# Kernel tuning notes

Hardware: AMD Instinct MI355X
Metric: run time of the kernel (lower is better)

Reference implementation:

```python
import jax, jax.numpy as jnp
import numpy as np
from jax import lax

B, T, IN, H, OUT, L = 256, 200, 128, 256, 118, 2


def _gru_layer(x_seq, Wih, Whh, bih, bhh):
    """x_seq: [B, T, D] -> all hidden states [B, T, H] (PyTorch GRU gate math)."""
    # Precompute input contribution to gates for all timesteps: [B, T, 3H]
    gx_all = jnp.einsum('btd,gd->btg', x_seq, Wih) + bih

    def step(h, gx):
        gh = h @ Whh.T + bhh                      # [B, 3H]
        r = jax.nn.sigmoid(gx[:, :H] + gh[:, :H])
        z = jax.nn.sigmoid(gx[:, H:2 * H] + gh[:, H:2 * H])
        n = jnp.tanh(gx[:, 2 * H:] + r * gh[:, 2 * H:])
        h_new = (1.0 - z) * n + z * h
        return h_new, h_new

    h0 = jnp.zeros((x_seq.shape[0], H), dtype=x_seq.dtype)
    _, hs = lax.scan(step, h0, gx_all.swapaxes(0, 1))  # hs: [T, B, H]
    return hs.swapaxes(0, 1)


def setup_inputs() -> dict:
    key = jax.random.key(0)
    ks = jax.random.split(key, 11)
    s_in = 1.0 / np.sqrt(H)
    u = lambda k, shp: jax.random.uniform(k, shp, jnp.float32, -s_in, s_in)
    return {
        'x':    jax.random.normal(ks[0], (B, T, IN), jnp.float32),
        'Wih0': u(ks[1], (3 * H, IN)),
        'Whh0': u(ks[2], (3 * H, H)),
        'bih0': u(ks[3], (3 * H,)),
        'bhh0': u(ks[4], (3 * H,)),
        'Wih1': u(ks[5], (3 * H, H)),
        'Whh1': u(ks[6], (3 * H, H)),
        'bih1': u(ks[7], (3 * H,)),
        'bhh1': u(ks[8], (3 * H,)),
        'fcW':  u(ks[9], (OUT, H)),
        'fcb':  u(ks[10], (OUT,)),
    }


def reference(x, Wih0, Whh0, bih0, bhh0, Wih1, Whh1, bih1, bhh1, fcW, fcb):
    h1 = _gru_layer(x, Wih0, Whh0, bih0, bhh0)   # [B, T, H]
    h2 = _gru_layer(h1, Wih1, Whh1, bih1, bhh1)  # [B, T, H]
    last = h2[:, -1, :]                           # out[:, -1, :]
    return last @ fcW.T + fcb                     # [B, OUT]
```

## Files before the change

kernel.cpp:

```cpp
#include <hip/hip_runtime.h>
#include <hip/hip_bf16.h>
#include <stdint.h>

#define BATCH 256
#define SEQT  200
#define IND   128
#define HID   256
#define G3    768
#define OUTD  118

#define TC    25
#define NC    8

#define HSTRIDE 264
#define W0SZ (G3*IND)
#define WHSZ (G3*HID)
#define XSZ  (BATCH*SEQT*IND)

#define SLOT_F  (BATCH*TC*G3)
#define SLOTP_F (SLOT_F + 2048)

#define NLOG2E (-1.44269504f)
#define LOG2E2 2.88539008f

typedef short  short8 __attribute__((ext_vector_type(8)));
typedef float  f32x4  __attribute__((ext_vector_type(4)));
typedef int    i32x4  __attribute__((ext_vector_type(4)));

__device__ __forceinline__ float exp2fast(float x) {
#if __has_builtin(__builtin_amdgcn_exp2f)
    return __builtin_amdgcn_exp2f(x);
#else
    return exp2f(x);
#endif
}

__device__ __forceinline__ unsigned short f2bf(float x) {
    union { float f; uint32_t u; } v; v.f = x;
    uint32_t u = v.u;
    u += 0x7FFF + ((u >> 16) & 1);
    return (unsigned short)(u >> 16);
}

__device__ __forceinline__ void scan_barrier() {
    asm volatile("s_waitcnt lgkmcnt(0)" ::: "memory");
    __builtin_amdgcn_s_barrier();
    __builtin_amdgcn_sched_barrier(0);
}

__global__ void cvt_all(const float* __restrict__ x,
                        const float* __restrict__ w0,  const float* __restrict__ wh0,
                        const float* __restrict__ w1,  const float* __restrict__ wh1,
                        unsigned short* __restrict__ xb,
                        unsigned short* __restrict__ o0,  unsigned short* __restrict__ oh0,
                        unsigned short* __restrict__ o1,  unsigned short* __restrict__ oh1) {
    const int n4 = (XSZ + W0SZ + 3 * WHSZ) / 4;
    int idx = blockIdx.x * blockDim.x + threadIdx.x;
    int stride = gridDim.x * blockDim.x;
    for (int i = idx; i < n4; i += stride) {
        int j = i * 4;
        const float* src; unsigned short* dst;
        if (j < XSZ) { src = x; dst = xb; }
        else {
            j -= XSZ;
            if (j < W0SZ) { src = w0; dst = o0; }
            else {
                j -= W0SZ;
                if (j < WHSZ) { src = wh0; dst = oh0; }
                else {
                    j -= WHSZ;
                    if (j < WHSZ) { src = w1; dst = o1; }
                    else { j -= WHSZ; src = wh1; dst = oh1; }
                }
            }
        }
        float4 v = *(const float4*)(src + j);
        ushort4 o;
        o.x = f2bf(v.x); o.y = f2bf(v.y); o.z = f2bf(v.z); o.w = f2bf(v.w);
        *(ushort4*)(dst + j) = o;
    }
}

__global__ void combine_bias(const float* __restrict__ bih0, const float* __restrict__ bhh0,
                             const float* __restrict__ bih1, const float* __restrict__ bhh1,
                             float* __restrict__ bc0, float* __restrict__ bc1) {
    int i = blockIdx.x * blockDim.x + threadIdx.x;
    if (i < G3) bc0[i] = bih0[i] + (i < 2 * HID ? bhh0[i] : 0.0f);
    else if (i < 2 * G3) {
        int j = i - G3;
        bc1[j] = bih1[j] + (j < 2 * HID ? bhh1[j] : 0.0f);
    }
}

template<int K>
__device__ __forceinline__ void g_stage(i32x4* sA, int tile, int t0,
    const unsigned short* A, const unsigned short* Bt, const float* bias,
    int tidu, short8 (&b)[2][8], float& bia0, float& bia1, int& g0o)
{
    constexpr int KS = K / 32, CPR = K / 8, LSTR = CPR + 1, PT = 128 * CPR / 256;
    const int wave = tidu >> 6, lane = tidu & 63, col = lane & 15, quad = lane >> 4;
    const int nb = tile % 6, panel = tile / 6;
    const int g0 = nb * 128 + wave * 32 + col;
    g0o = g0;
#pragma unroll
    for (int jt = 0; jt < 2; jt++)
#pragma unroll
        for (int ks = 0; ks < KS; ks++)
            b[jt][ks] = *(const short8*)(Bt + (size_t)(g0 + jt * 16) * K + ks * 32 + quad * 8);
    bia0 = bias[g0]; bia1 = bias[g0 + 16];

    i32x4 st[PT];
#pragma unroll
    for (int i = 0; i < PT; i++) {
        int g = i * 256 + tidu;
        int row = g / CPR, cc = g % CPR;
        int r = panel * 128 + row;
        int bb = r / TC, lt = r - bb * TC;
        st[i] = *(const i32x4*)(A + (size_t)(bb * SEQT + t0 + lt) * K + cc * 8);
    }
#pragma unroll
    for (int i = 0; i < PT; i++) {
        int g = i * 256 + tidu;
        sA[(g / CPR) * LSTR + (g % CPR)] = st[i];
    }
}

template<int K>
__device__ __forceinline__ void g_comp(const i32x4* sA, int tile,
    const short8 (&b)[2][8], float bia0, float bia1, int g0,
    float* Cslot, int tidu)
{
    constexpr int KS = K / 32, CPR = K / 8, LSTR = CPR + 1;
    const int lane = tidu & 63, col = lane & 15, quad = lane >> 4;
    const int nb = tile % 6, panel = tile / 6;
    const float scl = (nb < 4) ? NLOG2E : LOG2E2;
#pragma unroll 2
    for (int ms = 0; ms < 8; ms++) {
        f32x4 a0 = (f32x4)(0.0f), a1 = (f32x4)(0.0f);
#pragma unroll
        for (int ks = 0; ks < KS; ks++) {
            short8 a = __builtin_bit_cast(short8, sA[(ms * 16 + col) * LSTR + ks * 4 + quad]);
            a0 = __builtin_amdgcn_mfma_f32_16x16x32_bf16(a, b[0][ks], a0, 0, 0, 0);
            a1 = __builtin_amdgcn_mfma_f32_16x16x32_bf16(a, b[1][ks], a1, 0, 0, 0);
        }
        float* crow = Cslot + (size_t)(panel * 128 + ms * 16 + quad * 4) * G3 + g0;
#pragma unroll
        for (int r = 0; r < 4; r++) {
            crow[(size_t)r * G3]      = (a0[r] + bia0) * scl;
            crow[(size_t)r * G3 + 16] = (a1[r] + bia1) * scl;
        }
    }
}

__global__ __launch_bounds__(512, 2) void pipe(
    int c,
    const unsigned short* xb,
    unsigned short* h1b,
    const unsigned short* w0b, const unsigned short* w1b,
    const float* bc0, const float* bc1,
    float* gx0, float* gx1,
    const unsigned short* wh0, const unsigned short* wh1,
    const float* bhh0, const float* bhh1,
    float* hst0, float* hst1)
{
    __shared__ __attribute__((aligned(16))) char SM[16896 + 135168];

    const int bid = blockIdx.x;
    const int tid = threadIdx.x;

    if (bid < 128) {
        const bool L0 = bid < 64;
        const int cs = L0 ? c - 1 : c - 3;
        if (cs < 0 || cs >= NC) return;
        const float* gxslot = (L0 ? gx0 : gx1) + (size_t)(cs & 1) * SLOTP_F;
        const unsigned short* Whh = L0 ? wh0 : wh1;
        const float* bhh = L0 ? bhh0 : bhh1;
        float* hstate = L0 ? hst0 : hst1;
        unsigned short* h1o = L0 ? h1b : nullptr;
        const int wg = L0 ? bid : bid - 64;

        unsigned short* hs = (unsigned short*)SM;

        const int wave = tid >> 6, lane = tid & 63;
        const int col = lane & 15, quad = lane >> 4;
        const int jbase = wave * 32, j0 = jbase + col, j1 = jbase + 16 + col;
        const int bq  = wg * 4 + quad;
        const int row = quad * 4;

        i32x4 wrz[2][2][8];
#pragma unroll
        for (int g = 0; g < 2; g++)
#pragma unroll
            for (int jt = 0; jt < 2; jt++)
#pragma unroll
                for (int ks = 0; ks < 8; ks++)
                    wrz[g][jt][ks] = *(const i32x4*)(
                        Whh + (size_t)(g * HID + jbase + jt * 16 + col) * HID + ks * 32 + quad * 8);
        i32x4 wn0[8], wn1r[8];
#pragma unroll
        for (int ks = 0; ks < 8; ks++) {
            wn0[ks]  = *(const i32x4*)(Whh + (size_t)(2 * HID + j0) * HID + ks * 32 + quad * 8);
            wn1r[ks] = *(const i32x4*)(Whh + (size_t)(2 * HID + j1) * HID + ks * 32 + quad * 8);
        }

        for (int i = tid; i < 2 * 16 * HSTRIDE; i += 512) hs[i] = 0;

        float hreg[2];
        if (cs == 0) { hreg[0] = 0.0f; hreg[1] = 0.0f; }
        else {
            hreg[0] = hstate[bq * HID + j0];
            hreg[1] = hstate[bq * HID + j1];
        }
        float bhn[2] = { bhh[2 * HID + j0], bhh[2 * HID + j1] };

        __syncthreads();
        hs[row * HSTRIDE + j0] = f2bf(hreg[0]);
        hs[row * HSTRIDE + j1] = f2bf(hreg[1]);
        __syncthreads();

        int gof = (bq * TC) * G3 + j0;
        int hof = (bq * SEQT + cs * TC) * HID + j0;
        const int abase = col * HSTRIDE + quad * 8;
        const int wbase = row * HSTRIDE + j0;

        float gc[3][2], gc1[3][2], gc2[3][2];
#pragma unroll
        for (int g3 = 0; g3 < 3; g3++) {
            gc[g3][0] = gxslot[gof + g3 * HID];
            gc[g3][1] = gxslot[gof + g3 * HID + 16];
        }
        gof += G3;
#pragma unroll
        for (int g3 = 0; g3 < 3; g3++) {
            gc1[g3][0] = gxslot[gof + g3 * HID];
            gc1[g3][1] = gxslot[gof + g3 * HID + 16];
        }
        gof += G3;

        for (int lt = 0; lt < TC; lt++) {
            unsigned short* hc = hs + (lt & 1) * 16 * HSTRIDE;
            unsigned short* hn = hs + ((lt & 1) ^ 1) * 16 * HSTRIDE;

#pragma unroll
            for (int g = 0; g < 2; g++)
#pragma unroll
                for (int jt = 0; jt < 2; jt++)
#pragma unroll
                    for (int ks = 0; ks < 8; ks++)
                        asm volatile("" : "+v"(wrz[g][jt][ks]));
#pragma unroll
            for (int ks = 0; ks < 8; ks++) {
                asm volatile("" : "+v"(wn0[ks]));
                asm volatile("" : "+v"(wn1r[ks]));
            }

#pragma unroll
            for (int g3 = 0; g3 < 3; g3++) {
                gc2[g3][0] = gxslot[gof + g3 * HID];
                gc2[g3][1] = gxslot[gof + g3 * HID + 16];
            }
            gof += G3;

            f32x4 acc[3][2];
#pragma unroll
            for (int g = 0; g < 3; g++)
#pragma unroll
                for (int jt = 0; jt < 2; jt++) acc[g][jt] = (f32x4)(0.0f);

            __builtin_amdgcn_s_setprio(1);
#pragma unroll
            for (int ks = 0; ks < 8; ks++) {
                short8 a = *(const short8*)(&hc[abase + ks * 32]);
                acc[0][0] = __builtin_amdgcn_mfma_f32_16x16x32_bf16(a, __builtin_bit_cast(short8, wrz[0][0][ks]), acc[0][0], 0, 0, 0);
                acc[0][1] = __builtin_amdgcn_mfma_f32_16x16x32_bf16(a, __builtin_bit_cast(short8, wrz[0][1][ks]), acc[0][1], 0, 0, 0);
                acc[1][0] = __builtin_amdgcn_mfma_f32_16x16x32_bf16(a, __builtin_bit_cast(short8, wrz[1][0][ks]), acc[1][0], 0, 0, 0);
                acc[1][1] = __builtin_amdgcn_mfma_f32_16x16x32_bf16(a, __builtin_bit_cast(short8, wrz[1][1][ks]), acc[1][1], 0, 0, 0);
                acc[2][0] = __builtin_amdgcn_mfma_f32_16x16x32_bf16(a, __builtin_bit_cast(short8, wn0[ks]),       acc[2][0], 0, 0, 0);
                acc[2][1] = __builtin_amdgcn_mfma_f32_16x16x32_bf16(a, __builtin_bit_cast(short8, wn1r[ks]),      acc[2][1], 0, 0, 0);
            }
            __builtin_amdgcn_s_setprio(0);

            unsigned short hb[2];
#pragma unroll
            for (int jt = 0; jt < 2; jt++) {
                float er = exp2fast(__builtin_fmaf(acc[0][jt][0], NLOG2E, gc[0][jt]));
                float rr = __builtin_amdgcn_rcpf(1.0f + er);
                float ez = exp2fast(__builtin_fmaf(acc[1][jt][0], NLOG2E, gc[1][jt]));
                float zz = __builtin_amdgcn_rcpf(1.0f + ez);
                float inner = acc[2][jt][0] + bhn[jt];
                float en = exp2fast(__builtin_fmaf(rr * inner, LOG2E2, gc[2][jt]));
                float nn = __builtin_fmaf(__builtin_amdgcn_rcpf(1.0f + en), -2.0f, 1.0f);
                float hnew = __builtin_fmaf(zz, hreg[jt] - nn, nn);
                hreg[jt] = hnew;
                hb[jt] = f2bf(hnew);
                hn[wbase + jt * 16] = hb[jt];
            }

            if (h1o) {
                h1o[hof]      = hb[0];
                h1o[hof + 16] = hb[1];
            }
            hof += HID;

#pragma unroll
            for (int g3 = 0; g3 < 3; g3++) {
                gc[g3][0]  = gc1[g3][0];  gc[g3][1]  = gc1[g3][1];
                gc1[g3][0] = gc2[g3][0];  gc1[g3][1] = gc2[g3][1];
            }

            scan_barrier();
        }

        hstate[bq * HID + j0] = hreg[0];
        hstate[bq * HID + j1] = hreg[1];

    } else {
        const int cg0 = c, cg1 = c - 2;
        const int G0t = (cg0 < NC) ? 300 : 0;
        const int G1t = (cg1 >= 0 && cg1 < NC) ? 300 : 0;
        if (G0t + G1t == 0) return;

        i32x4* sA = (i32x4*)(SM + 16896) + (tid >> 8) * 4224;
        const int u    = (bid - 128) * 2 + (tid >> 8);
        const int tidu = tid & 255;
        float* c0slot = gx0 + (size_t)(cg0 & 1) * SLOTP_F;
        float* c1slot = gx1 + (size_t)(cg1 & 1) * SLOTP_F;

        short8 bf[2][8];
        float bia0, bia1; int g0c;

#pragma unroll 1
        for (int it = 0; it < 3; it++) {
            int t = it * 256 + u;
            int mode = (t < G0t) ? 0 : ((t - G0t < G1t) ? 1 : -1);
            int tile = (mode == 1) ? t - G0t : t;
            if (mode == 0)
                g_stage<IND>(sA, tile, cg0 * TC, xb, w0b, bc0, tidu, bf, bia0, bia1, g0c);
            else if (mode == 1)
                g_stage<HID>(sA, tile, cg1 * TC, h1b, w1b, bc1, tidu, bf, bia0, bia1, g0c);
            __syncthreads();
            if (mode == 0)
                g_comp<IND>(sA, tile, bf, bia0, bia1, g0c, c0slot, tidu);
            else if (mode == 1)
                g_comp<HID>(sA, tile, bf, bia0, bia1, g0c, c1slot, tidu);
            __syncthreads();
        }
    }
}

__global__ __launch_bounds__(128) void fc_kernel(
    const float* __restrict__ hlast, const float* __restrict__ W,
    const float* __restrict__ b, float* __restrict__ out)
{
    __shared__ float hsm[HID];
    int bidx = blockIdx.x;
    for (int i = threadIdx.x; i < HID; i += 128) hsm[i] = hlast[(size_t)bidx * HID + i];
    __syncthreads();
    int o = threadIdx.x;
    if (o < OUTD) {
        float acc = b[o];
        const float* wrow = W + (size_t)o * HID;
#pragma unroll 4
        for (int k = 0; k < HID; k++) acc += hsm[k] * wrow[k];
        out[(size_t)bidx * OUTD + o] = acc;
    }
}

extern "C" void kernel_launch(void* const* d_in, const int* in_sizes, int n_in,
                              void* d_out, int out_size, void* d_ws, size_t ws_size,
                              hipStream_t stream) {
    const float* x    = (const float*)d_in[0];
    const float* Wih0 = (const float*)d_in[1];
    const float* Whh0 = (const float*)d_in[2];
    const float* bih0 = (const float*)d_in[3];
    const float* bhh0 = (const float*)d_in[4];
    const float* Wih1 = (const float*)d_in[5];
    const float* Whh1 = (const float*)d_in[6];
    const float* bih1 = (const float*)d_in[7];
    const float* bhh1 = (const float*)d_in[8];
    const float* fcW  = (const float*)d_in[9];
    const float* fcb  = (const float*)d_in[10];
    float* out = (float*)d_out;

    char* ws = (char*)d_ws;
    size_t off = 0;
    auto walloc = [&](size_t bytes) {
        void* p = ws + off;
        off = (off + bytes + 255) & ~(size_t)255;
        return p;
    };

    const int M = BATCH * SEQT;
    unsigned short* xb   = (unsigned short*)walloc((size_t)XSZ * 2);
    float*          gx0  = (float*)         walloc((size_t)2 * SLOTP_F * 4);
    float*          gx1  = (float*)         walloc((size_t)2 * SLOTP_F * 4);
    unsigned short* h1b  = (unsigned short*)walloc((size_t)M * HID * 2);
    unsigned short* w0b  = (unsigned short*)walloc((size_t)W0SZ * 2);
    unsigned short* wh0b = (unsigned short*)walloc((size_t)WHSZ * 2);
    unsigned short* w1b  = (unsigned short*)walloc((size_t)WHSZ * 2);
    unsigned short* wh1b = (unsigned short*)walloc((size_t)WHSZ * 2);
    float*          bc0  = (float*)         walloc(G3 * 4);
    float*          bc1  = (float*)         walloc(G3 * 4);
    float*          hst0 = (float*)         walloc((size_t)BATCH * HID * 4);
    float*          hst1 = (float*)         walloc((size_t)BATCH * HID * 4);

    cvt_all     <<<2048, 256, 0, stream>>>(x, Wih0, Whh0, Wih1, Whh1,
                                           xb, w0b, wh0b, w1b, wh1b);
    combine_bias<<<6,    256, 0, stream>>>(bih0, bhh0, bih1, bhh1, bc0, bc1);

    for (int c = 0; c <= NC + 2; ++c)
        pipe<<<256, 512, 0, stream>>>(c, xb, h1b, w0b, w1b, bc0, bc1,
                                      gx0, gx1, wh0b, wh1b, bhh0, bhh1, hst0, hst1);

    fc_kernel<<<BATCH, 128, 0, stream>>>(hst1, fcW, fcb, out);
}
```

Baseline: 506.9 us.

## Replace per-chunk kernel launches with persistent kernel using flag-based inter-block sync

Folds the eleven chunk-pipeline launches into one persistent kernel. Recurrence blocks keep their hidden state and weights in registers across chunks. Blocks coordinate through global atomic counters: recurrence blocks spin until the input-projection tiles for their chunk are published, and GEMM blocks wait for the h1 and slot-reuse completion counts before writing. This removes launch gaps and the hidden-state save/restore through global memory between chunks. In exchange it adds spin-wait latency and coherent atomic loads, and it relies on all 256 blocks being co-resident to avoid deadlock.

```diff
diff --git a/kernel.cpp b/kernel.cpp
--- a/kernel.cpp
+++ b/kernel.cpp
@@ -11,6 +11,7 @@
 
 #define TC    25
 #define NC    8
+#define G0TILES 300
 
 #define HSTRIDE 264
 #define W0SZ (G3*IND)
@@ -19,6 +20,11 @@
 
 #define SLOT_F  (BATCH*TC*G3)
 #define SLOTP_F (SLOT_F + 2048)
+
+#define FH1 0
+#define FS1 8
+#define FG0 16
+#define FG1 24
 
 #define NLOG2E (-1.44269504f)
 #define LOG2E2 2.88539008f
@@ -48,14 +54,28 @@
     __builtin_amdgcn_sched_barrier(0);
 }
 
+__device__ __forceinline__ void spin_ge(int* p, int tgt) {
+    while (__hip_atomic_load(p, __ATOMIC_ACQUIRE, __HIP_MEMORY_SCOPE_AGENT) < tgt)
+        __builtin_amdgcn_s_sleep(2);
+}
+
+__device__ __forceinline__ float gloadf(const float* p) {
+    return __hip_atomic_load(p, __ATOMIC_RELAXED, __HIP_MEMORY_SCOPE_AGENT);
+}
+__device__ __forceinline__ uint32_t gloadu(const uint32_t* p) {
+    return __hip_atomic_load(p, __ATOMIC_RELAXED, __HIP_MEMORY_SCOPE_AGENT);
+}
+
 __global__ void cvt_all(const float* __restrict__ x,
                         const float* __restrict__ w0,  const float* __restrict__ wh0,
                         const float* __restrict__ w1,  const float* __restrict__ wh1,
                         unsigned short* __restrict__ xb,
                         unsigned short* __restrict__ o0,  unsigned short* __restrict__ oh0,
-                        unsigned short* __restrict__ o1,  unsigned short* __restrict__ oh1) {
+                        unsigned short* __restrict__ o1,  unsigned short* __restrict__ oh1,
+                        int* __restrict__ flg) {
     const int n4 = (XSZ + W0SZ + 3 * WHSZ) / 4;
     int idx = blockIdx.x * blockDim.x + threadIdx.x;
+    if (idx < 32) flg[idx] = 0;
     int stride = gridDim.x * blockDim.x;
     for (int i = idx; i < n4; i += stride) {
         int j = i * 4;
@@ -92,7 +112,7 @@
     }
 }
 
-template<int K>
+template<int K, bool COH>
 __device__ __forceinline__ void g_stage(i32x4* sA, int tile, int t0,
     const unsigned short* A, const unsigned short* Bt, const float* bias,
     int tidu, short8 (&b)[2][8], float& bia0, float& bia1, int& g0o)
@@ -116,7 +136,18 @@
         int row = g / CPR, cc = g % CPR;
         int r = panel * 128 + row;
         int bb = r / TC, lt = r - bb * TC;
-        st[i] = *(const i32x4*)(A + (size_t)(bb * SEQT + t0 + lt) * K + cc * 8);
+        const unsigned short* src = A + (size_t)(bb * SEQT + t0 + lt) * K + cc * 8;
+        if constexpr (COH) {
+            const uint32_t* q = (const uint32_t*)src;
+            i32x4 v;
+            v[0] = (int)gloadu(q + 0);
+            v[1] = (int)gloadu(q + 1);
+            v[2] = (int)gloadu(q + 2);
+            v[3] = (int)gloadu(q + 3);
+            st[i] = v;
+        } else {
+            st[i] = *(const i32x4*)src;
+        }
     }
 #pragma unroll
     for (int i = 0; i < PT; i++) {
@@ -152,8 +183,7 @@
     }
 }
 
-__global__ __launch_bounds__(512, 2) void pipe(
-    int c,
+__global__ __launch_bounds__(512, 2) void persist(
     const unsigned short* xb,
     unsigned short* h1b,
     const unsigned short* w0b, const unsigned short* w1b,
@@ -161,7 +191,7 @@
     float* gx0, float* gx1,
     const unsigned short* wh0, const unsigned short* wh1,
     const float* bhh0, const float* bhh1,
-    float* hst0, float* hst1)
+    float* hlast, int* flg)
 {
     __shared__ __attribute__((aligned(16))) char SM[16896 + 135168];
 
@@ -170,14 +200,13 @@
 
     if (bid < 128) {
         const bool L0 = bid < 64;
-        const int cs = L0 ? c - 1 : c - 3;
-        if (cs < 0 || cs >= NC) return;
-        const float* gxslot = (L0 ? gx0 : gx1) + (size_t)(cs & 1) * SLOTP_F;
         const unsigned short* Whh = L0 ? wh0 : wh1;
         const float* bhh = L0 ? bhh0 : bhh1;
-        float* hstate = L0 ? hst0 : hst1;
+        float* gxb = L0 ? gx0 : gx1;
         unsigned short* h1o = L0 ? h1b : nullptr;
         const int wg = L0 ? bid : bid - 64;
+        int* fgx   = flg + (L0 ? FG0 : FG1);
+        int* fdone = flg + (L0 ? FH1 : FS1);
 
         unsigned short* hs = (unsigned short*)SM;
 
@@ -205,145 +234,174 @@
 
         for (int i = tid; i < 2 * 16 * HSTRIDE; i += 512) hs[i] = 0;
 
-        float hreg[2];
-        if (cs == 0) { hreg[0] = 0.0f; hreg[1] = 0.0f; }
-        else {
-            hreg[0] = hstate[bq * HID + j0];
-            hreg[1] = hstate[bq * HID + j1];
-        }
+        float hreg[2] = { 0.0f, 0.0f };
         float bhn[2] = { bhh[2 * HID + j0], bhh[2 * HID + j1] };
-
-        __syncthreads();
-        hs[row * HSTRIDE + j0] = f2bf(hreg[0]);
-        hs[row * HSTRIDE + j1] = f2bf(hreg[1]);
-        __syncthreads();
-
-        int gof = (bq * TC) * G3 + j0;
-        int hof = (bq * SEQT + cs * TC) * HID + j0;
         const int abase = col * HSTRIDE + quad * 8;
         const int wbase = row * HSTRIDE + j0;
 
-        float gc[3][2], gc1[3][2], gc2[3][2];
-#pragma unroll
-        for (int g3 = 0; g3 < 3; g3++) {
-            gc[g3][0] = gxslot[gof + g3 * HID];
-            gc[g3][1] = gxslot[gof + g3 * HID + 16];
-        }
-        gof += G3;
-#pragma unroll
-        for (int g3 = 0; g3 < 3; g3++) {
-            gc1[g3][0] = gxslot[gof + g3 * HID];
-            gc1[g3][1] = gxslot[gof + g3 * HID + 16];
-        }
-        gof += G3;
-
-        for (int lt = 0; lt < TC; lt++) {
-            unsigned short* hc = hs + (lt & 1) * 16 * HSTRIDE;
-            unsigned short* hn = hs + ((lt & 1) ^ 1) * 16 * HSTRIDE;
-
-#pragma unroll
-            for (int g = 0; g < 2; g++)
-#pragma unroll
-                for (int jt = 0; jt < 2; jt++)
-#pragma unroll
-                    for (int ks = 0; ks < 8; ks++)
-                        asm volatile("" : "+v"(wrz[g][jt][ks]));
-#pragma unroll
-            for (int ks = 0; ks < 8; ks++) {
-                asm volatile("" : "+v"(wn0[ks]));
-                asm volatile("" : "+v"(wn1r[ks]));
-            }
-
+        __syncthreads();
+
+        int cur = 0;
+        for (int c = 0; c < NC; ++c) {
+            if (tid == 0) spin_ge(&fgx[c], G0TILES);
+            __syncthreads();
+
+            const float* gxslot = gxb + (size_t)(c & 1) * SLOTP_F;
+            int gof = (bq * TC) * G3 + j0;
+            int hof = (bq * SEQT + c * TC) * HID + j0;
+
+            float gc[3][2], gc1[3][2], gc2[3][2];
 #pragma unroll
             for (int g3 = 0; g3 < 3; g3++) {
-                gc2[g3][0] = gxslot[gof + g3 * HID];
-                gc2[g3][1] = gxslot[gof + g3 * HID + 16];
+                gc[g3][0] = gloadf(gxslot + gof + g3 * HID);
+                gc[g3][1] = gloadf(gxslot + gof + g3 * HID + 16);
             }
             gof += G3;
-
-            f32x4 acc[3][2];
-#pragma unroll
-            for (int g = 0; g < 3; g++)
-#pragma unroll
-                for (int jt = 0; jt < 2; jt++) acc[g][jt] = (f32x4)(0.0f);
-
-            __builtin_amdgcn_s_setprio(1);
-#pragma unroll
-            for (int ks = 0; ks < 8; ks++) {
-                short8 a = *(const short8*)(&hc[abase + ks * 32]);
-                acc[0][0] = __builtin_amdgcn_mfma_f32_16x16x32_bf16(a, __builtin_bit_cast(short8, wrz[0][0][ks]), acc[0][0], 0, 0, 0);
-                acc[0][1] = __builtin_amdgcn_mfma_f32_16x16x32_bf16(a, __builtin_bit_cast(short8, wrz[0][1][ks]), acc[0][1], 0, 0, 0);
-                acc[1][0] = __builtin_amdgcn_mfma_f32_16x16x32_bf16(a, __builtin_bit_cast(short8, wrz[1][0][ks]), acc[1][0], 0, 0, 0);
-                acc[1][1] = __builtin_amdgcn_mfma_f32_16x16x32_bf16(a, __builtin_bit_cast(short8, wrz[1][1][ks]), acc[1][1], 0, 0, 0);
-                acc[2][0] = __builtin_amdgcn_mfma_f32_16x16x32_bf16(a, __builtin_bit_cast(short8, wn0[ks]),       acc[2][0], 0, 0, 0);
-                acc[2][1] = __builtin_amdgcn_mfma_f32_16x16x32_bf16(a, __builtin_bit_cast(short8, wn1r[ks]),      acc[2][1], 0, 0, 0);
-            }
-            __builtin_amdgcn_s_setprio(0);
-
-            unsigned short hb[2];
-#pragma unroll
-            for (int jt = 0; jt < 2; jt++) {
-                float er = exp2fast(__builtin_fmaf(acc[0][jt][0], NLOG2E, gc[0][jt]));
-                float rr = __builtin_amdgcn_rcpf(1.0f + er);
-                float ez = exp2fast(__builtin_fmaf(acc[1][jt][0], NLOG2E, gc[1][jt]));
-                float zz = __builtin_amdgcn_rcpf(1.0f + ez);
-                float inner = acc[2][jt][0] + bhn[jt];
-                float en = exp2fast(__builtin_fmaf(rr * inner, LOG2E2, gc[2][jt]));
-                float nn = __builtin_fmaf(__builtin_amdgcn_rcpf(1.0f + en), -2.0f, 1.0f);
-                float hnew = __builtin_fmaf(zz, hreg[jt] - nn, nn);
-                hreg[jt] = hnew;
-                hb[jt] = f2bf(hnew);
-                hn[wbase + jt * 16] = hb[jt];
-            }
-
-            if (h1o) {
-                h1o[hof]      = hb[0];
-                h1o[hof + 16] = hb[1];
-            }
-            hof += HID;
-
 #pragma unroll
             for (int g3 = 0; g3 < 3; g3++) {
-                gc[g3][0]  = gc1[g3][0];  gc[g3][1]  = gc1[g3][1];
-                gc1[g3][0] = gc2[g3][0];  gc1[g3][1] = gc2[g3][1];
-            }
-
-            scan_barrier();
-        }
-
-        hstate[bq * HID + j0] = hreg[0];
-        hstate[bq * HID + j1] = hreg[1];
+                gc1[g3][0] = gloadf(gxslot + gof + g3 * HID);
+                gc1[g3][1] = gloadf(gxslot + gof + g3 * HID + 16);
+            }
+            gof += G3;
+
+            for (int lt = 0; lt < TC; lt++) {
+                unsigned short* hc = hs + cur * 16 * HSTRIDE;
+                unsigned short* hn = hs + (cur ^ 1) * 16 * HSTRIDE;
+
+#pragma unroll
+                for (int g = 0; g < 2; g++)
+#pragma unroll
+                    for (int jt = 0; jt < 2; jt++)
+#pragma unroll
+                        for (int ks = 0; ks < 8; ks++)
+                            asm volatile("" : "+v"(wrz[g][jt][ks]));
+#pragma unroll
+                for (int ks = 0; ks < 8; ks++) {
+                    asm volatile("" : "+v"(wn0[ks]));
+                    asm volatile("" : "+v"(wn1r[ks]));
+                }
+
+#pragma unroll
+                for (int g3 = 0; g3 < 3; g3++) {
+                    gc2[g3][0] = gloadf(gxslot + gof + g3 * HID);
+                    gc2[g3][1] = gloadf(gxslot + gof + g3 * HID + 16);
+                }
+                gof += G3;
+
+                f32x4 acc[3][2];
+#pragma unroll
+                for (int g = 0; g < 3; g++)
+#pragma unroll
+                    for (int jt = 0; jt < 2; jt++) acc[g][jt] = (f32x4)(0.0f);
+
+                __builtin_amdgcn_s_setprio(1);
+#pragma unroll
+                for (int ks = 0; ks < 8; ks++) {
+                    short8 a = *(const short8*)(&hc[abase + ks * 32]);
+                    acc[0][0] = __builtin_amdgcn_mfma_f32_16x16x32_bf16(a, __builtin_bit_cast(short8, wrz[0][0][ks]), acc[0][0], 0, 0, 0);
+                    acc[0][1] = __builtin_amdgcn_mfma_f32_16x16x32_bf16(a, __builtin_bit_cast(short8, wrz[0][1][ks]), acc[0][1], 0, 0, 0);
+                    acc[1][0] = __builtin_amdgcn_mfma_f32_16x16x32_bf16(a, __builtin_bit_cast(short8, wrz[1][0][ks]), acc[1][0], 0, 0, 0);
+                    acc[1][1] = __builtin_amdgcn_mfma_f32_16x16x32_bf16(a, __builtin_bit_cast(short8, wrz[1][1][ks]), acc[1][1], 0, 0, 0);
+                    acc[2][0] = __builtin_amdgcn_mfma_f32_16x16x32_bf16(a, __builtin_bit_cast(short8, wn0[ks]),       acc[2][0], 0, 0, 0);
+                    acc[2][1] = __builtin_amdgcn_mfma_f32_16x16x32_bf16(a, __builtin_bit_cast(short8, wn1r[ks]),      acc[2][1], 0, 0, 0);
+                }
+                __builtin_amdgcn_s_setprio(0);
+
+                unsigned short hb[2];
+#pragma unroll
+                for (int jt = 0; jt < 2; jt++) {
+                    float er = exp2fast(__builtin_fmaf(acc[0][jt][0], NLOG2E, gc[0][jt]));
+                    float rr = __builtin_amdgcn_rcpf(1.0f + er);
+                    float ez = exp2fast(__builtin_fmaf(acc[1][jt][0], NLOG2E, gc[1][jt]));
+                    float zz = __builtin_amdgcn_rcpf(1.0f + ez);
+                    float inner = acc[2][jt][0] + bhn[jt];
+                    float en = exp2fast(__builtin_fmaf(rr * inner, LOG2E2, gc[2][jt]));
+                    float nn = __builtin_fmaf(__builtin_amdgcn_rcpf(1.0f + en), -2.0f, 1.0f);
+                    float hnew = __builtin_fmaf(zz, hreg[jt] - nn, nn);
+                    hreg[jt] = hnew;
+                    hb[jt] = f2bf(hnew);
+                    hn[wbase + jt * 16] = hb[jt];
+                }
+
+                if (h1o) {
+                    h1o[hof]      = hb[0];
+                    h1o[hof + 16] = hb[1];
+                }
+                hof += HID;
+
+#pragma unroll
+                for (int g3 = 0; g3 < 3; g3++) {
+                    gc[g3][0]  = gc1[g3][0];  gc[g3][1]  = gc1[g3][1];
+                    gc1[g3][0] = gc2[g3][0];  gc1[g3][1] = gc2[g3][1];
+                }
+
+                cur ^= 1;
+                scan_barrier();
+            }
+
+            __threadfence();
+            __syncthreads();
+            if (tid == 0)
+                __hip_atomic_fetch_add(&fdone[c], 1, __ATOMIC_RELEASE, __HIP_MEMORY_SCOPE_AGENT);
+        }
+
+        if (!L0) {
+            hlast[bq * HID + j0]      = hreg[0];
+            hlast[bq * HID + j0 + 16] = hreg[1];
+        }
 
     } else {
-        const int cg0 = c, cg1 = c - 2;
-        const int G0t = (cg0 < NC) ? 300 : 0;
-        const int G1t = (cg1 >= 0 && cg1 < NC) ? 300 : 0;
-        if (G0t + G1t == 0) return;
-
+        const int g  = bid - 128;
+        const int uu = g * 2 + (tid >> 8);
+        const int tidu = tid & 255;
+        const int ub = uu * G0TILES / 256;
+        const int ue = (uu + 1) * G0TILES / 256;
         i32x4* sA = (i32x4*)(SM + 16896) + (tid >> 8) * 4224;
-        const int u    = (bid - 128) * 2 + (tid >> 8);
-        const int tidu = tid & 255;
-        float* c0slot = gx0 + (size_t)(cg0 & 1) * SLOTP_F;
-        float* c1slot = gx1 + (size_t)(cg1 & 1) * SLOTP_F;
+
+        const int blkTiles = ((g * 2 + 2) * G0TILES / 256) - ((g * 2) * G0TILES / 256);
 
         short8 bf[2][8];
         float bia0, bia1; int g0c;
 
+        for (int cc = 0; cc < NC + 2; ++cc) {
+            const int c0 = cc, c1 = cc - 2;
+            const bool do0 = (c0 < NC), do1 = (c1 >= 0);
+
+            if (tid == 0) {
+                if (do0 && c0 >= 2) spin_ge(&flg[FH1 + c0 - 2], 64);
+                if (do1) {
+                    spin_ge(&flg[FH1 + c1], 64);
+                    if (c1 >= 2) spin_ge(&flg[FS1 + c1 - 2], 64);
+                }
+            }
+            __syncthreads();
+
+            float* s0 = gx0 + (size_t)(c0 & 1) * SLOTP_F;
+            float* s1 = gx1 + (size_t)(c1 & 1) * SLOTP_F;
+
 #pragma unroll 1
-        for (int it = 0; it < 3; it++) {
-            int t = it * 256 + u;
-            int mode = (t < G0t) ? 0 : ((t - G0t < G1t) ? 1 : -1);
-            int tile = (mode == 1) ? t - G0t : t;
-            if (mode == 0)
-                g_stage<IND>(sA, tile, cg0 * TC, xb, w0b, bc0, tidu, bf, bia0, bia1, g0c);
-            else if (mode == 1)
-                g_stage<HID>(sA, tile, cg1 * TC, h1b, w1b, bc1, tidu, bf, bia0, bia1, g0c);
+            for (int r = 0; r < 2; ++r) {
+                int t = ub + r; bool act = do0 && (t < ue);
+                if (act) g_stage<IND, false>(sA, t, c0 * TC, xb, w0b, bc0, tidu, bf, bia0, bia1, g0c);
+                __syncthreads();
+                if (act) g_comp<IND>(sA, t, bf, bia0, bia1, g0c, s0, tidu);
+                __syncthreads();
+            }
+#pragma unroll 1
+            for (int r = 0; r < 2; ++r) {
+                int t = ub + r; bool act = do1 && (t < ue);
+                if (act) g_stage<HID, true>(sA, t, c1 * TC, h1b, w1b, bc1, tidu, bf, bia0, bia1, g0c);
+                __syncthreads();
+                if (act) g_comp<HID>(sA, t, bf, bia0, bia1, g0c, s1, tidu);
+                __syncthreads();
+            }
+
+            __threadfence();
             __syncthreads();
-            if (mode == 0)
-                g_comp<IND>(sA, tile, bf, bia0, bia1, g0c, c0slot, tidu);
-            else if (mode == 1)
-                g_comp<HID>(sA, tile, bf, bia0, bia1, g0c, c1slot, tidu);
-            __syncthreads();
+            if (tid == 0) {
+                if (do0) __hip_atomic_fetch_add(&flg[FG0 + c0], blkTiles, __ATOMIC_RELEASE, __HIP_MEMORY_SCOPE_AGENT);
+                if (do1) __hip_atomic_fetch_add(&flg[FG1 + c1], blkTiles, __ATOMIC_RELEASE, __HIP_MEMORY_SCOPE_AGENT);
+            }
         }
     }
 }
@@ -401,16 +459,16 @@
     unsigned short* wh1b = (unsigned short*)walloc((size_t)WHSZ * 2);
     float*          bc0  = (float*)         walloc(G3 * 4);
     float*          bc1  = (float*)         walloc(G3 * 4);
-    float*          hst0 = (float*)         walloc((size_t)BATCH * HID * 4);
-    float*          hst1 = (float*)         walloc((size_t)BATCH * HID * 4);
+    float*          hlast= (float*)         walloc((size_t)BATCH * HID * 4);
+    int*            flg  = (int*)           walloc(32 * 4);
 
     cvt_all     <<<2048, 256, 0, stream>>>(x, Wih0, Whh0, Wih1, Whh1,
-                                           xb, w0b, wh0b, w1b, wh1b);
+                                           xb, w0b, wh0b, w1b, wh1b, flg);
     combine_bias<<<6,    256, 0, stream>>>(bih0, bhh0, bih1, bhh1, bc0, bc1);
 
-    for (int c = 0; c <= NC + 2; ++c)
-        pipe<<<256, 512, 0, stream>>>(c, xb, h1b, w0b, w1b, bc0, bc1,
-                                      gx0, gx1, wh0b, wh1b, bhh0, bhh1, hst0, hst1);
-
-    fc_kernel<<<BATCH, 128, 0, stream>>>(hst1, fcW, fcb, out);
-}
+    persist<<<256, 512, 0, stream>>>(xb, h1b, w0b, w1b, bc0, bc1,
+                                     gx0, gx1, wh0b, wh1b, bhh0, bhh1,
+                                     hlast, flg);
+
+    fc_kernel<<<BATCH, 128, 0, stream>>>(hlast, fcW, fcb, out);
+}
```

Measured after the change: 1.557 ms. 3.07x slower.
